# Performance work log

Measured on AMD Instinct MI355X. Metric: run time of the kernel, lower is better.

The kernel has to match this reference:

```python
import jax, jax.numpy as jnp
import numpy as np

MARGIN = 0.5


def setup_inputs() -> dict:
    key = jax.random.key(0)
    k1, k2, k3, k4, k5 = jax.random.split(key, 5)
    N, V, D = 4096, 10000, 128
    return {
        "context_batch": jax.random.normal(k1, (N, V), dtype=jnp.float32),
        "response_batch": jax.random.normal(k2, (N, V), dtype=jnp.float32),
        "neg_response_batch": jax.random.normal(k3, (N, V), dtype=jnp.float32),
        # uniform(-1, 1) init as in reset_parameters
        "context_embedding": jax.random.uniform(k4, (D, V), minval=-1.0, maxval=1.0, dtype=jnp.float32),
        "response_embedding": jax.random.uniform(k5, (D, V), minval=-1.0, maxval=1.0, dtype=jnp.float32),
    }


def reference(context_batch, response_batch, neg_response_batch,
              context_embedding, response_embedding):
    # cont_rep: [N, D] = (E_c @ X^T)^T
    cont_rep = context_batch @ context_embedding.T          # [N, D]
    resp_rep = response_batch @ response_embedding.T        # [N, D]
    neg_resp_rep = neg_response_batch @ response_embedding.T  # [N, D]
    # diag(cont_rep @ resp_rep^T) == row-wise dot product (same math, O(N*D))
    f_pos = jnp.sum(cont_rep * resp_rep, axis=-1)           # [N]
    f_neg = jnp.sum(cont_rep * neg_resp_rep, axis=-1)       # [N]
    loss = jnp.sum(jax.nn.relu(f_neg - f_pos + MARGIN))
    return f_pos, f_neg, loss
```

## Files before the change

kernel.cpp:

```cpp
#include <hip/hip_runtime.h>
#include <hip/hip_bf16.h>
#include <cstdint>

#define VDIM 10000
#define VPAD 10016
#define NROW 4096
#define DDIM 128
#define KSTEPS 313
#define KSPLIT 8
#define KCHUNK 40

typedef __attribute__((ext_vector_type(8))) short bf16x8;
typedef __attribute__((ext_vector_type(4))) float f32x4;

__device__ __forceinline__ unsigned short f2bf(float f) {
    union { float f; unsigned u; } v; v.f = f;
    unsigned u = v.u;
    unsigned r = (u + 0x7FFFu + ((u >> 16) & 1u)) >> 16;
    return (unsigned short)r;
}

__global__ __launch_bounds__(256) void convert_emb(
    const float* __restrict__ ec, const float* __restrict__ er,
    unsigned short* __restrict__ out)
{
    int idx8 = (blockIdx.x * 256 + threadIdx.x) * 8;
    const int total = 2 * DDIM * VPAD;
    if (idx8 >= total) return;
    int e   = idx8 / (DDIM * VPAD);
    int rem = idx8 - e * (DDIM * VPAD);
    int row = rem / VPAD;
    int k   = rem - row * VPAD;
    unsigned short o[8];
    if (k < VDIM) {
        const float* src = (e ? er : ec) + row * VDIM + k;
        #pragma unroll
        for (int j = 0; j < 8; ++j) o[j] = f2bf(src[j]);
    } else {
        #pragma unroll
        for (int j = 0; j < 8; ++j) o[j] = 0;
    }
    *reinterpret_cast<bf16x8*>(out + idx8) = *reinterpret_cast<const bf16x8*>(o);
}

__global__ __launch_bounds__(256, 3) void gemm_rep(
    const float* __restrict__ a0, const float* __restrict__ a1,
    const float* __restrict__ a2,
    const unsigned short* __restrict__ emb,
    float* __restrict__ reps)
{
    __shared__ short bLds[2][DDIM][40];

    const int rb = blockIdx.x;
    const int s  = blockIdx.y;
    const int kc = blockIdx.z;
    const float* A = (s == 0) ? a0 : (s == 1 ? a1 : a2);
    const unsigned short* E = emb + (size_t)(s == 0 ? 0 : 1) * (DDIM * VPAD);

    const int tid  = threadIdx.x;
    const int wave = tid >> 6;
    const int lane = tid & 63;
    const int l15  = lane & 15;
    const int quad = lane >> 4;

    const int scol  = tid >> 1;
    const int shalf = tid & 1;
    const unsigned short* sp = E + (size_t)scol * VPAD + shalf * 16;

    const int kt0 = kc * KCHUNK;
    const int kt1 = (kt0 + KCHUNK < KSTEPS) ? (kt0 + KCHUNK) : KSTEPS;

    const int r0 = rb * 128 + wave * 32;
    const float* ap0 = A + (size_t)(r0 + l15) * VDIM;
    const float* ap1 = A + (size_t)(r0 + 16 + l15) * VDIM;

    f32x4 acc[2][8];
    #pragma unroll
    for (int rf = 0; rf < 2; ++rf)
        #pragma unroll
        for (int ct = 0; ct < 8; ++ct) acc[rf][ct] = (f32x4){0.f, 0.f, 0.f, 0.f};

    bf16x8 s0a, s0b, s1a, s1b;

#define GLOADB(sa, sb, KT) do {                                        \
        const unsigned short* q_ = sp + (size_t)(KT) * 32;             \
        sa = *reinterpret_cast<const bf16x8*>(q_);                     \
        sb = *reinterpret_cast<const bf16x8*>(q_ + 8);                 \
    } while (0)

#define DSWRITE(BUF, sa, sb) do {                                      \
        *reinterpret_cast<bf16x8*>(&bLds[BUF][scol][shalf * 16])     = sa; \
        *reinterpret_cast<bf16x8*>(&bLds[BUF][scol][shalf * 16 + 8]) = sb; \
    } while (0)

#define COMPUTE(KT, BUF) do {                                          \
        const int koct_ = (KT) * 32 + quad * 8;                        \
        bf16x8 af0 = (bf16x8){0,0,0,0,0,0,0,0};                        \
        bf16x8 af1 = (bf16x8){0,0,0,0,0,0,0,0};                        \
        if (koct_ < VDIM) {                                            \
            const f32x4 f0 = *reinterpret_cast<const f32x4*>(ap0 + koct_);     \
            const f32x4 f1 = *reinterpret_cast<const f32x4*>(ap0 + koct_ + 4); \
            const f32x4 g0 = *reinterpret_cast<const f32x4*>(ap1 + koct_);     \
            const f32x4 g1 = *reinterpret_cast<const f32x4*>(ap1 + koct_ + 4); \
            af0[0]=(short)f2bf(f0[0]); af0[1]=(short)f2bf(f0[1]);      \
            af0[2]=(short)f2bf(f0[2]); af0[3]=(short)f2bf(f0[3]);      \
            af0[4]=(short)f2bf(f1[0]); af0[5]=(short)f2bf(f1[1]);      \
            af0[6]=(short)f2bf(f1[2]); af0[7]=(short)f2bf(f1[3]);      \
            af1[0]=(short)f2bf(g0[0]); af1[1]=(short)f2bf(g0[1]);      \
            af1[2]=(short)f2bf(g0[2]); af1[3]=(short)f2bf(g0[3]);      \
            af1[4]=(short)f2bf(g1[0]); af1[5]=(short)f2bf(g1[1]);      \
            af1[6]=(short)f2bf(g1[2]); af1[7]=(short)f2bf(g1[3]);      \
        }                                                              \
        bf16x8 bfr[8];                                                 \
        _Pragma("unroll")                                              \
        for (int ct = 0; ct < 8; ++ct)                                 \
            bfr[ct] = *reinterpret_cast<const bf16x8*>(                \
                &bLds[BUF][ct * 16 + l15][quad * 8]);                  \
        _Pragma("unroll")                                              \
        for (int ct = 0; ct < 8; ++ct) {                               \
            acc[0][ct] = __builtin_amdgcn_mfma_f32_16x16x32_bf16(af0, bfr[ct], acc[0][ct], 0, 0, 0); \
            acc[1][ct] = __builtin_amdgcn_mfma_f32_16x16x32_bf16(af1, bfr[ct], acc[1][ct], 0, 0, 0); \
        }                                                              \
    } while (0)

    GLOADB(s0a, s0b, kt0);
    int kt = kt0;
    while (true) {
        if (kt + 1 < kt1) GLOADB(s1a, s1b, kt + 1);
        DSWRITE(0, s0a, s0b);
        __syncthreads();
        COMPUTE(kt, 0);
        if (++kt >= kt1) break;
        if (kt + 1 < kt1) GLOADB(s0a, s0b, kt + 1);
        DSWRITE(1, s1a, s1b);
        __syncthreads();
        COMPUTE(kt, 1);
        if (++kt >= kt1) break;
    }

    float* rp = reps + (size_t)s * NROW * DDIM + (size_t)r0 * DDIM;
    #pragma unroll
    for (int rf = 0; rf < 2; ++rf)
        #pragma unroll
        for (int ct = 0; ct < 8; ++ct)
            #pragma unroll
            for (int r = 0; r < 4; ++r)
                atomicAdd(rp + (size_t)(rf * 16 + quad * 4 + r) * DDIM + ct * 16 + l15,
                          acc[rf][ct][r]);
#undef GLOADB
#undef DSWRITE
#undef COMPUTE
}

__global__ __launch_bounds__(256) void finalize(
    const float* __restrict__ reps, float* __restrict__ out)
{
    __shared__ float ls[4];
    const int wid  = threadIdx.x >> 6;
    const int lane = threadIdx.x & 63;
    const int row  = blockIdx.x * 4 + wid;

    const float* c = reps + (size_t)row * DDIM + 2 * lane;
    const float* r = c + (size_t)NROW * DDIM;
    const float* n = r + (size_t)NROW * DDIM;
    const float2 cv = *reinterpret_cast<const float2*>(c);
    const float2 rv = *reinterpret_cast<const float2*>(r);
    const float2 nv = *reinterpret_cast<const float2*>(n);

    float fp = cv.x * rv.x + cv.y * rv.y;
    float fn = cv.x * nv.x + cv.y * nv.y;
    #pragma unroll
    for (int off = 32; off > 0; off >>= 1) {
        fp += __shfl_down(fp, off);
        fn += __shfl_down(fn, off);
    }
    if (lane == 0) {
        out[row]        = fp;
        out[NROW + row] = fn;
        float t = fn - fp + 0.5f;
        ls[wid] = t > 0.f ? t : 0.f;
    }
    __syncthreads();
    if (threadIdx.x == 0)
        atomicAdd(out + 2 * NROW, ls[0] + ls[1] + ls[2] + ls[3]);
}

extern "C" void kernel_launch(void* const* d_in, const int* in_sizes, int n_in,
                              void* d_out, int out_size, void* d_ws, size_t ws_size,
                              hipStream_t stream)
{
    const float* cb  = (const float*)d_in[0];
    const float* rbb = (const float*)d_in[1];
    const float* nb  = (const float*)d_in[2];
    const float* ce  = (const float*)d_in[3];
    const float* re  = (const float*)d_in[4];
    float* out = (float*)d_out;

    unsigned short* emb = (unsigned short*)d_ws;
    const size_t embBytes = (size_t)2 * DDIM * VPAD * sizeof(unsigned short);
    float* reps = (float*)((char*)d_ws + embBytes);
    const size_t repBytes = (size_t)3 * NROW * DDIM * sizeof(float);

    convert_emb<<<dim3((2 * DDIM * VPAD / 8) / 256), dim3(256), 0, stream>>>(ce, re, emb);
    hipMemsetAsync(reps, 0, repBytes, stream);
    hipMemsetAsync(out + 2 * NROW, 0, sizeof(float), stream);
    gemm_rep<<<dim3(NROW / 128, 3, KSPLIT), dim3(256), 0, stream>>>(cb, rbb, nb, emb, reps);
    finalize<<<dim3(NROW / 4), dim3(256), 0, stream>>>(reps, out);
}
```

Measured before the change: 178.8 us.

## Deepen GEMM software pipeline with register-prefetched A and single barrier per step

Result: slower. 207.3 us (+16.0%).

```diff
diff --git a/kernel.cpp b/kernel.cpp
--- a/kernel.cpp
+++ b/kernel.cpp
@@ -80,7 +80,11 @@
         #pragma unroll
         for (int ct = 0; ct < 8; ++ct) acc[rf][ct] = (f32x4){0.f, 0.f, 0.f, 0.f};
 
-    bf16x8 s0a, s0b, s1a, s1b;
+    bf16x8 sA0, sA1, sB0, sB1;
+    f32x4 ar0, ar1, ar2, ar3;
+    bf16x8 af0, af1;
+
+#define CLAMPK(KT) (((KT) < KSTEPS - 1) ? (KT) : (KSTEPS - 1))
 
 #define GLOADB(sa, sb, KT) do {                                        \
         const unsigned short* q_ = sp + (size_t)(KT) * 32;             \
@@ -88,53 +92,85 @@
         sb = *reinterpret_cast<const bf16x8*>(q_ + 8);                 \
     } while (0)
 
+#define GLOADA(KT) do {                                                \
+        int koA_ = (KT) * 32 + quad * 8;                               \
+        int koC_ = koA_ > (VDIM - 8) ? (VDIM - 8) : koA_;              \
+        ar0 = *reinterpret_cast<const f32x4*>(ap0 + koC_);             \
+        ar1 = *reinterpret_cast<const f32x4*>(ap0 + koC_ + 4);         \
+        ar2 = *reinterpret_cast<const f32x4*>(ap1 + koC_);             \
+        ar3 = *reinterpret_cast<const f32x4*>(ap1 + koC_ + 4);         \
+    } while (0)
+
+#define CONVA(KT) do {                                                 \
+        int ko_ = (KT) * 32 + quad * 8;                                \
+        if (ko_ < VDIM) {                                              \
+            af0[0]=(short)f2bf(ar0[0]); af0[1]=(short)f2bf(ar0[1]);    \
+            af0[2]=(short)f2bf(ar0[2]); af0[3]=(short)f2bf(ar0[3]);    \
+            af0[4]=(short)f2bf(ar1[0]); af0[5]=(short)f2bf(ar1[1]);    \
+            af0[6]=(short)f2bf(ar1[2]); af0[7]=(short)f2bf(ar1[3]);    \
+            af1[0]=(short)f2bf(ar2[0]); af1[1]=(short)f2bf(ar2[1]);    \
+            af1[2]=(short)f2bf(ar2[2]); af1[3]=(short)f2bf(ar2[3]);    \
+            af1[4]=(short)f2bf(ar3[0]); af1[5]=(short)f2bf(ar3[1]);    \
+            af1[6]=(short)f2bf(ar3[2]); af1[7]=(short)f2bf(ar3[3]);    \
+        } else {                                                       \
+            af0 = (bf16x8){0,0,0,0,0,0,0,0};                           \
+            af1 = (bf16x8){0,0,0,0,0,0,0,0};                           \
+        }                                                              \
+    } while (0)
+
 #define DSWRITE(BUF, sa, sb) do {                                      \
         *reinterpret_cast<bf16x8*>(&bLds[BUF][scol][shalf * 16])     = sa; \
         *reinterpret_cast<bf16x8*>(&bLds[BUF][scol][shalf * 16 + 8]) = sb; \
     } while (0)
 
-#define COMPUTE(KT, BUF) do {                                          \
-        const int koct_ = (KT) * 32 + quad * 8;                        \
-        bf16x8 af0 = (bf16x8){0,0,0,0,0,0,0,0};                        \
-        bf16x8 af1 = (bf16x8){0,0,0,0,0,0,0,0};                        \
-        if (koct_ < VDIM) {                                            \
-            const f32x4 f0 = *reinterpret_cast<const f32x4*>(ap0 + koct_);     \
-            const f32x4 f1 = *reinterpret_cast<const f32x4*>(ap0 + koct_ + 4); \
-            const f32x4 g0 = *reinterpret_cast<const f32x4*>(ap1 + koct_);     \
-            const f32x4 g1 = *reinterpret_cast<const f32x4*>(ap1 + koct_ + 4); \
-            af0[0]=(short)f2bf(f0[0]); af0[1]=(short)f2bf(f0[1]);      \
-            af0[2]=(short)f2bf(f0[2]); af0[3]=(short)f2bf(f0[3]);      \
-            af0[4]=(short)f2bf(f1[0]); af0[5]=(short)f2bf(f1[1]);      \
-            af0[6]=(short)f2bf(f1[2]); af0[7]=(short)f2bf(f1[3]);      \
-            af1[0]=(short)f2bf(g0[0]); af1[1]=(short)f2bf(g0[1]);      \
-            af1[2]=(short)f2bf(g0[2]); af1[3]=(short)f2bf(g0[3]);      \
-            af1[4]=(short)f2bf(g1[0]); af1[5]=(short)f2bf(g1[1]);      \
-            af1[6]=(short)f2bf(g1[2]); af1[7]=(short)f2bf(g1[3]);      \
-        }                                                              \
-        bf16x8 bfr[8];                                                 \
-        _Pragma("unroll")                                              \
-        for (int ct = 0; ct < 8; ++ct)                                 \
-            bfr[ct] = *reinterpret_cast<const bf16x8*>(                \
-                &bLds[BUF][ct * 16 + l15][quad * 8]);                  \
-        _Pragma("unroll")                                              \
-        for (int ct = 0; ct < 8; ++ct) {                               \
-            acc[0][ct] = __builtin_amdgcn_mfma_f32_16x16x32_bf16(af0, bfr[ct], acc[0][ct], 0, 0, 0); \
-            acc[1][ct] = __builtin_amdgcn_mfma_f32_16x16x32_bf16(af1, bfr[ct], acc[1][ct], 0, 0, 0); \
-        }                                                              \
-    } while (0)
-
-    GLOADB(s0a, s0b, kt0);
+#define BODY(T, P, Sa, Sb) do {                                        \
+        CONVA(T);                       \
+        GLOADA((T) + 1);                \
+        DSWRITE((P) ^ 1, Sa, Sb);        \
+        GLOADB(Sa, Sb, CLAMPK((T) + 3));   \
+        bf16x8 b0_ = *reinterpret_cast<const bf16x8*>(&bLds[P][ 0 + l15][quad * 8]); \
+        bf16x8 b1_ = *reinterpret_cast<const bf16x8*>(&bLds[P][16 + l15][quad * 8]); \
+        bf16x8 b2_ = *reinterpret_cast<const bf16x8*>(&bLds[P][32 + l15][quad * 8]); \
+        bf16x8 b3_ = *reinterpret_cast<const bf16x8*>(&bLds[P][48 + l15][quad * 8]); \
+        acc[0][0] = __builtin_amdgcn_mfma_f32_16x16x32_bf16(af0, b0_, acc[0][0], 0, 0, 0); \
+        acc[1][0] = __builtin_amdgcn_mfma_f32_16x16x32_bf16(af1, b0_, acc[1][0], 0, 0, 0); \
+        acc[0][1] = __builtin_amdgcn_mfma_f32_16x16x32_bf16(af0, b1_, acc[0][1], 0, 0, 0); \
+        acc[1][1] = __builtin_amdgcn_mfma_f32_16x16x32_bf16(af1, b1_, acc[1][1], 0, 0, 0); \
+        acc[0][2] = __builtin_amdgcn_mfma_f32_16x16x32_bf16(af0, b2_, acc[0][2], 0, 0, 0); \
+        acc[1][2] = __builtin_amdgcn_mfma_f32_16x16x32_bf16(af1, b2_, acc[1][2], 0, 0, 0); \
+        acc[0][3] = __builtin_amdgcn_mfma_f32_16x16x32_bf16(af0, b3_, acc[0][3], 0, 0, 0); \
+        acc[1][3] = __builtin_amdgcn_mfma_f32_16x16x32_bf16(af1, b3_, acc[1][3], 0, 0, 0); \
+        bf16x8 b4_ = *reinterpret_cast<const bf16x8*>(&bLds[P][ 64 + l15][quad * 8]); \
+        bf16x8 b5_ = *reinterpret_cast<const bf16x8*>(&bLds[P][ 80 + l15][quad * 8]); \
+        bf16x8 b6_ = *reinterpret_cast<const bf16x8*>(&bLds[P][ 96 + l15][quad * 8]); \
+        bf16x8 b7_ = *reinterpret_cast<const bf16x8*>(&bLds[P][112 + l15][quad * 8]); \
+        acc[0][4] = __builtin_amdgcn_mfma_f32_16x16x32_bf16(af0, b4_, acc[0][4], 0, 0, 0); \
+        acc[1][4] = __builtin_amdgcn_mfma_f32_16x16x32_bf16(af1, b4_, acc[1][4], 0, 0, 0); \
+        acc[0][5] = __builtin_amdgcn_mfma_f32_16x16x32_bf16(af0, b5_, acc[0][5], 0, 0, 0); \
+        acc[1][5] = __builtin_amdgcn_mfma_f32_16x16x32_bf16(af1, b5_, acc[1][5], 0, 0, 0); \
+        acc[0][6] = __builtin_amdgcn_mfma_f32_16x16x32_bf16(af0, b6_, acc[0][6], 0, 0, 0); \
+        acc[1][6] = __builtin_amdgcn_mfma_f32_16x16x32_bf16(af1, b6_, acc[1][6], 0, 0, 0); \
+        acc[0][7] = __builtin_amdgcn_mfma_f32_16x16x32_bf16(af0, b7_, acc[0][7], 0, 0, 0); \
+        acc[1][7] = __builtin_amdgcn_mfma_f32_16x16x32_bf16(af1, b7_, acc[1][7], 0, 0, 0); \
+        asm volatile("s_barrier" ::: "memory");                        \
+    } while (0)
+
+    {
+        bf16x8 p0_, p1_;
+        GLOADB(p0_, p1_, kt0);
+        DSWRITE(0, p0_, p1_);
+        GLOADB(sA0, sA1, CLAMPK(kt0 + 1));
+        GLOADB(sB0, sB1, CLAMPK(kt0 + 2));
+        GLOADA(kt0);
+        asm volatile("s_waitcnt lgkmcnt(0)" ::: "memory");
+        asm volatile("s_barrier" ::: "memory");
+    }
+
     int kt = kt0;
     while (true) {
-        if (kt + 1 < kt1) GLOADB(s1a, s1b, kt + 1);
-        DSWRITE(0, s0a, s0b);
-        __syncthreads();
-        COMPUTE(kt, 0);
+        BODY(kt, 0, sA0, sA1);
         if (++kt >= kt1) break;
-        if (kt + 1 < kt1) GLOADB(s0a, s0b, kt + 1);
-        DSWRITE(1, s1a, s1b);
-        __syncthreads();
-        COMPUTE(kt, 1);
+        BODY(kt, 1, sB0, sB1);
         if (++kt >= kt1) break;
     }
 
@@ -147,9 +183,12 @@
             for (int r = 0; r < 4; ++r)
                 atomicAdd(rp + (size_t)(rf * 16 + quad * 4 + r) * DDIM + ct * 16 + l15,
                           acc[rf][ct][r]);
+#undef BODY
+#undef DSWRITE
+#undef CONVA
+#undef GLOADA
 #undef GLOADB
-#undef DSWRITE
-#undef COMPUTE
+#undef CLAMPK
 }
 
 __global__ __launch_bounds__(256) void finalize(
```
